# Performance work log

Measured on AMD Instinct MI355X. Metric: run time of the kernel, lower is better.

The kernel has to match this reference:

```python
import jax, jax.numpy as jnp
import numpy as np
import math

S, B, E, H = 2048, 2, 1024, 16
D = E // H
LN_EPS = 1e-5


def setup_inputs() -> dict:
    key = jax.random.key(0)
    ks = jax.random.split(key, 8)
    src = jax.random.normal(ks[0], (S, B, E), dtype=jnp.float32)
    # causal attention mask: 1 = attend, 0 = masked
    src_mask = jnp.tril(jnp.ones((S, S), dtype=jnp.int32))
    in_proj_w = jax.random.normal(ks[1], (2 * E, E), dtype=jnp.float32) * 0.02
    in_proj_b = jnp.zeros((2 * E,), dtype=jnp.float32)
    out_proj_w = jax.random.normal(ks[2], (E, E), dtype=jnp.float32) * 0.02
    out_proj_b = jnp.zeros((E,), dtype=jnp.float32)
    ln_g = jnp.ones((E,), dtype=jnp.float32)
    ln_b = jnp.zeros((E,), dtype=jnp.float32)
    return {"src": src, "src_mask": src_mask, "in_proj_w": in_proj_w,
            "in_proj_b": in_proj_b, "out_proj_w": out_proj_w,
            "out_proj_b": out_proj_b, "ln_g": ln_g, "ln_b": ln_b}


def _layernorm(x, g, b):
    mu = jnp.mean(x, axis=-1, keepdims=True)
    var = jnp.mean(jnp.square(x - mu), axis=-1, keepdims=True)
    return (x - mu) * jax.lax.rsqrt(var + LN_EPS) * g + b


def reference(src, src_mask, in_proj_w, in_proj_b, out_proj_w, out_proj_b, ln_g, ln_b):
    # src: (S, B, E)
    x_norm = _layernorm(src, ln_g, ln_b)
    proj = jax.nn.silu(x_norm @ in_proj_w.T + in_proj_b)     # (S, B, 2E)
    qkv, u = jnp.split(proj, 2, axis=-1)                     # each (S, B, E)
    qkv = qkv.reshape(S, B, H, D)                            # q = k = v = qkv
    # scores: (B, H, S_q, S_k)
    scores = jnp.einsum('sbhd,tbhd->bhst', qkv, qkv) / math.sqrt(D)
    # torch does masked_fill(-inf) then silu; silu(-inf) -> 0 in the limit,
    # which is the intended semantics (masked positions contribute nothing).
    weights = jnp.where(src_mask[None, None, :, :] == 0, 0.0, jax.nn.silu(scores))
    # attn_dropout is identity at eval
    attn = jnp.einsum('bhst,tbhd->sbhd', weights, qkv).reshape(S, B, E)
    gated = attn * u
    out = src + (gated @ out_proj_w.T + out_proj_b)          # out_dropout = identity
    return out
```

## Files before the change

### kernel.cpp

```cpp
#include <hip/hip_runtime.h>


typedef __attribute__((ext_vector_type(8))) short  short8;
typedef __attribute__((ext_vector_type(4))) float  floatx4;
typedef __attribute__((ext_vector_type(4))) float  fvec4;
typedef __attribute__((ext_vector_type(4))) unsigned short usvec4;
typedef __attribute__((ext_vector_type(4))) int    intx4;

__device__ __forceinline__ unsigned short f2b(float f) {
  unsigned u = __builtin_bit_cast(unsigned, f);
  u += 0x7FFFu + ((u >> 16) & 1u);
  return (unsigned short)(u >> 16);
}
__device__ __forceinline__ float b2f(unsigned short h) {
  unsigned u = ((unsigned)h) << 16;
  return __builtin_bit_cast(float, u);
}
__device__ __forceinline__ float silu_f(float x) {
  float e = __builtin_amdgcn_exp2f(-1.44269504f * x);
  return x * __builtin_amdgcn_rcpf(1.f + e);
}
__device__ __forceinline__ void async_copy16(void* lds, const void* g) {
  __builtin_amdgcn_global_load_lds(
      (__attribute__((address_space(1))) void*)(g),
      (__attribute__((address_space(3))) void*)(lds), 16, 0, 0);
}

__global__ void cvt_bf16(const float* __restrict__ s, unsigned short* __restrict__ d, int n4) {
  int i = blockIdx.x * 256 + threadIdx.x;
  if (i < n4) {
    fvec4 v = ((const fvec4*)s)[i];
    usvec4 o = { f2b(v.x), f2b(v.y), f2b(v.z), f2b(v.w) };
    ((usvec4*)d)[i] = o;
  }
}

__global__ __launch_bounds__(256) void ln_kernel(
    const float* __restrict__ x, const float* __restrict__ g,
    const float* __restrict__ b, unsigned short* __restrict__ xn) {
  const int row = blockIdx.x, t = threadIdx.x;
  const float* xr = x + (long)row * 1024;
  fvec4 v = ((const fvec4*)xr)[t];
  float s  = v.x + v.y + v.z + v.w;
  float s2 = v.x*v.x + v.y*v.y + v.z*v.z + v.w*v.w;
  #pragma unroll
  for (int off = 32; off; off >>= 1) { s += __shfl_down(s, off); s2 += __shfl_down(s2, off); }
  __shared__ float red[8];
  int lane = t & 63, w = t >> 6;
  if (lane == 0) { red[w] = s; red[4 + w] = s2; }
  __syncthreads();
  s  = red[0] + red[1] + red[2] + red[3];
  s2 = red[4] + red[5] + red[6] + red[7];
  float mu  = s * (1.f / 1024.f);
  float var = s2 * (1.f / 1024.f) - mu * mu;
  float rs  = rsqrtf(var + 1e-5f);
  fvec4 gg = ((const fvec4*)g)[t];
  fvec4 bb = ((const fvec4*)b)[t];
  usvec4 o = { f2b((v.x - mu) * rs * gg.x + bb.x),
               f2b((v.y - mu) * rs * gg.y + bb.y),
               f2b((v.z - mu) * rs * gg.z + bb.z),
               f2b((v.w - mu) * rs * gg.w + bb.w) };
  ((usvec4*)(xn + (long)row * 1024))[t] = o;
}

__global__ __launch_bounds__(256, 2) void gemm_in(
    const unsigned short* __restrict__ A, const unsigned short* __restrict__ Bw,
    const float* __restrict__ bias,
    unsigned short* __restrict__ out0, unsigned short* __restrict__ out1) {
  __shared__ __align__(16) unsigned short sA[128 * 32];
  __shared__ __align__(16) unsigned short sB[128 * 32];
  const int t = threadIdx.x;
  const int lane = t & 63, l15 = lane & 15, quad = lane >> 4;
  const int w = t >> 6, wm = w >> 1, wn = w & 1;
  const int m0 = blockIdx.y * 128, n0 = blockIdx.x * 128;
  const int K = 1024;

  floatx4 acc[4][4];
  const floatx4 z4 = {0.f, 0.f, 0.f, 0.f};
  #pragma unroll
  for (int i = 0; i < 4; i++)
    #pragma unroll
    for (int j = 0; j < 4; j++) acc[i][j] = z4;

  for (int kt = 0; kt < 32; ++kt) {
    const int k0 = kt << 5;
    __syncthreads();
    #pragma unroll
    for (int c = 0; c < 2; ++c) {
      int slot = c * 256 + t;
      int row = slot >> 2, col = (slot & 3) << 3;
      async_copy16(&sA[slot * 8], &A[(m0 + row) * K + k0 + col]);
      async_copy16(&sB[slot * 8], &Bw[(n0 + row) * K + k0 + col]);
    }
    __syncthreads();
    short8 af[4], bf[4];
    #pragma unroll
    for (int mr = 0; mr < 4; mr++)
      af[mr] = *(const short8*)&sA[(wm * 64 + mr * 16 + l15) * 32 + quad * 8];
    #pragma unroll
    for (int nr = 0; nr < 4; nr++)
      bf[nr] = *(const short8*)&sB[(wn * 64 + nr * 16 + l15) * 32 + quad * 8];
    #pragma unroll
    for (int mr = 0; mr < 4; mr++)
      #pragma unroll
      for (int nr = 0; nr < 4; nr++)
        acc[mr][nr] = __builtin_amdgcn_mfma_f32_16x16x32_bf16(af[mr], bf[nr], acc[mr][nr], 0, 0, 0);
  }

  #pragma unroll
  for (int mr = 0; mr < 4; mr++) {
    int gm0 = m0 + wm * 64 + mr * 16 + quad * 4;
    #pragma unroll
    for (int nr = 0; nr < 4; nr++) {
      int gn = n0 + wn * 64 + nr * 16 + l15;
      float bv = bias[gn];
      unsigned short* dst = (gn < 1024) ? (out0 + gn) : (out1 + gn - 1024);
      #pragma unroll
      for (int r = 0; r < 4; r++) {
        float v = acc[mr][nr][r] + bv;
        dst[(long)(gm0 + r) * 1024] = f2b(silu_f(v));
      }
    }
  }
}

__global__ __launch_bounds__(256, 2) void gemm_out(
    const unsigned short* __restrict__ A, const unsigned short* __restrict__ Bw,
    const float* __restrict__ bias, const float* __restrict__ src,
    float* __restrict__ outf) {
  __shared__ __align__(16) unsigned short sA[128 * 32];
  __shared__ __align__(16) unsigned short sB[64 * 32];
  const int t = threadIdx.x;
  const int lane = t & 63, l15 = lane & 15, quad = lane >> 4;
  const int w = t >> 6;
  const int m0 = blockIdx.y * 128, n0 = blockIdx.x * 64;

  floatx4 acc[2][4];
  const floatx4 z4 = {0.f, 0.f, 0.f, 0.f};
  #pragma unroll
  for (int i = 0; i < 2; i++)
    #pragma unroll
    for (int j = 0; j < 4; j++) acc[i][j] = z4;

  for (int kt = 0; kt < 32; ++kt) {
    const int k0 = kt << 5;
    __syncthreads();
    #pragma unroll
    for (int c = 0; c < 2; ++c) {
      int slot = c * 256 + t;
      int row = slot >> 2, col = (slot & 3) << 3;
      async_copy16(&sA[slot * 8], &A[(m0 + row) * 1024 + k0 + col]);
    }
    { int row = t >> 2, col = (t & 3) << 3;
      async_copy16(&sB[t * 8], &Bw[(n0 + row) * 1024 + k0 + col]); }
    __syncthreads();
    short8 af[2], bf[4];
    #pragma unroll
    for (int mr = 0; mr < 2; mr++)
      af[mr] = *(const short8*)&sA[(w * 32 + mr * 16 + l15) * 32 + quad * 8];
    #pragma unroll
    for (int nr = 0; nr < 4; nr++)
      bf[nr] = *(const short8*)&sB[(nr * 16 + l15) * 32 + quad * 8];
    #pragma unroll
    for (int mr = 0; mr < 2; mr++)
      #pragma unroll
      for (int nr = 0; nr < 4; nr++)
        acc[mr][nr] = __builtin_amdgcn_mfma_f32_16x16x32_bf16(af[mr], bf[nr], acc[mr][nr], 0, 0, 0);
  }

  #pragma unroll
  for (int mr = 0; mr < 2; mr++) {
    int gm0 = m0 + w * 32 + mr * 16 + quad * 4;
    #pragma unroll
    for (int nr = 0; nr < 4; nr++) {
      int gn = n0 + nr * 16 + l15;
      float bv = bias[gn];
      #pragma unroll
      for (int r = 0; r < 4; r++) {
        long idx = (long)(gm0 + r) * 1024 + gn;
        outf[idx] = acc[mr][nr][r] + bv + src[idx];
      }
    }
  }
}

#define SKS 72
#define SVS 136
#define SPS 136
#define SOS 68
__global__ __launch_bounds__(256, 4) void attn_kernel(
    const unsigned short* __restrict__ qkv, const unsigned short* __restrict__ u,
    unsigned short* __restrict__ gated) {
  __shared__ __align__(16) unsigned char smem[128 * SKS * 2 + 64 * SVS * 2];
  unsigned short* sK  = (unsigned short*)smem;
  unsigned short* sP  = (unsigned short*)smem;
  unsigned short* sVt = (unsigned short*)(smem + 128 * SKS * 2);
  float*          sO  = (float*)smem;

  const int t = threadIdx.x, lane = t & 63, l15 = lane & 15, quad = lane >> 4;
  const int w = t >> 6;
  const int gg = blockIdx.x >> 5, sub = gg >> 3, g = gg & 7;
  const int qi = (sub == 0) ? g : (sub == 1) ? (31 - g) : (sub == 2) ? (g + 8) : (23 - g);
  const int bh = blockIdx.x & 31;
  const int b = bh >> 4, h = bh & 15;
  const long base = (long)b * 1024 + h * 64;
  const int q0 = qi * 64;
  const int rg = t >> 3, dg = t & 7;
  const int swz0 = (rg >> 1) + dg;

  #pragma unroll
  for (int c = 0; c < 2; ++c) {
    int slot = c * 256 + t, row = slot >> 3, cg = slot & 7;
    *(short8*)&sK[row * SKS + cg * 8] =
        *(const short8*)&qkv[base + (long)(q0 + row) * 2048 + cg * 8];
  }
  __syncthreads();
  short8 qf[4][2];
  #pragma unroll
  for (int mr = 0; mr < 4; mr++)
    #pragma unroll
    for (int ks = 0; ks < 2; ks++)
      qf[mr][ks] = *(const short8*)&sK[(mr * 16 + l15) * SKS + ks * 32 + quad * 8];

  floatx4 oacc[4];
  const floatx4 z4 = {0.f, 0.f, 0.f, 0.f};
  #pragma unroll
  for (int i = 0; i < 4; i++) oacc[i] = z4;

  const int d_rd = w * 16 + l15;
  const int rsw0 = quad + (d_rd & 7) + (d_rd >> 3);

  const int nkt = (qi >> 1) + 1;
  short8 kv[4];
  #pragma unroll
  for (int i = 0; i < 4; ++i)
    kv[i] = *(const short8*)&qkv[base + (long)(rg * 4 + i) * 2048 + dg * 8];

  for (int kt = 0; kt < nkt; ++kt) {
    const int t0 = kt * 128;
    __syncthreads();
    #pragma unroll
    for (int i = 0; i < 4; ++i)
      *(short8*)&sK[(rg * 4 + i) * SKS + dg * 8] = kv[i];
    {
      intx4 k0 = __builtin_bit_cast(intx4, kv[0]);
      intx4 k1 = __builtin_bit_cast(intx4, kv[1]);
      intx4 k2 = __builtin_bit_cast(intx4, kv[2]);
      intx4 k3 = __builtin_bit_cast(intx4, kv[3]);
      #pragma unroll
      for (int jj = 0; jj < 4; ++jj) {
        unsigned lo = __builtin_amdgcn_perm((unsigned)k1[jj], (unsigned)k0[jj], 0x05040100u);
        unsigned hi = __builtin_amdgcn_perm((unsigned)k3[jj], (unsigned)k2[jj], 0x05040100u);
        int j = 2 * jj, d = dg * 8 + j;
        int gsw = (swz0 + j) & 15;
        *(unsigned long long*)&sVt[d * SVS + gsw * 8 + (rg & 1) * 4] =
            (unsigned long long)lo | ((unsigned long long)hi << 32);
        lo = __builtin_amdgcn_perm((unsigned)k1[jj], (unsigned)k0[jj], 0x07060302u);
        hi = __builtin_amdgcn_perm((unsigned)k3[jj], (unsigned)k2[jj], 0x07060302u);
        j = 2 * jj + 1; d = dg * 8 + j;
        gsw = (swz0 + j) & 15;
        *(unsigned long long*)&sVt[d * SVS + gsw * 8 + (rg & 1) * 4] =
            (unsigned long long)lo | ((unsigned long long)hi << 32);
      }
    }
    __syncthreads();
    if (kt + 1 < nkt) {
      const long nb = base + (long)((kt + 1) * 128) * 2048;
      #pragma unroll
      for (int i = 0; i < 4; ++i)
        kv[i] = *(const short8*)&qkv[nb + (long)(rg * 4 + i) * 2048 + dg * 8];
    }
    floatx4 sacc[4][2];
    #pragma unroll
    for (int i = 0; i < 4; i++) { sacc[i][0] = z4; sacc[i][1] = z4; }
    #pragma unroll
    for (int ks = 0; ks < 2; ++ks) {
      short8 kf[2];
      #pragma unroll
      for (int nr = 0; nr < 2; nr++)
        kf[nr] = *(const short8*)&sK[(w * 32 + nr * 16 + l15) * SKS + ks * 32 + quad * 8];
      #pragma unroll
      for (int mr = 0; mr < 4; mr++)
        #pragma unroll
        for (int nr = 0; nr < 2; nr++)
          sacc[mr][nr] = __builtin_amdgcn_mfma_f32_16x16x32_bf16(qf[mr][ks], kf[nr], sacc[mr][nr], 0, 0, 0);
    }
    const bool diag = (kt == nkt - 1);
    #pragma unroll
    for (int mr = 0; mr < 4; mr++) {
      int row0 = mr * 16 + quad * 4;
      #pragma unroll
      for (int nr = 0; nr < 2; nr++) {
        int col = w * 32 + nr * 16 + l15;
        #pragma unroll
        for (int r = 0; r < 4; r++) {
          float v = silu_f(sacc[mr][nr][r] * 0.125f);
          if (diag && (q0 + row0 + r < t0 + col)) v = 0.f;
          sacc[mr][nr][r] = v;
        }
      }
    }
    __syncthreads();
    #pragma unroll
    for (int mr = 0; mr < 4; mr++)
      #pragma unroll
      for (int nr = 0; nr < 2; nr++)
        #pragma unroll
        for (int r = 0; r < 4; r++)
          sP[(mr * 16 + quad * 4 + r) * SPS + w * 32 + nr * 16 + l15] = f2b(sacc[mr][nr][r]);
    __syncthreads();
    #pragma unroll
    for (int ts = 0; ts < 4; ++ts) {
      int gsw = (ts * 4 + rsw0) & 15;
      short8 vfr = *(const short8*)&sVt[d_rd * SVS + gsw * 8];
      #pragma unroll
      for (int mr = 0; mr < 4; mr++) {
        short8 pf = *(const short8*)&sP[(mr * 16 + l15) * SPS + ts * 32 + quad * 8];
        oacc[mr] = __builtin_amdgcn_mfma_f32_16x16x32_bf16(pf, vfr, oacc[mr], 0, 0, 0);
      }
    }
  }

  __syncthreads();
  #pragma unroll
  for (int mr = 0; mr < 4; mr++)
    #pragma unroll
    for (int r = 0; r < 4; r++)
      sO[(mr * 16 + quad * 4 + r) * SOS + w * 16 + l15] = oacc[mr][r];
  __syncthreads();
  {
    const int erow = t >> 2, edg = t & 3;
    const float* sOr = sO + erow * SOS + edg * 16;
    const long grow = (long)(q0 + erow) * 2048 + base + edg * 16;
    short8 u0 = *(const short8*)&u[grow];
    short8 u1 = *(const short8*)&u[grow + 8];
    short8 g0, g1;
    #pragma unroll
    for (int j = 0; j < 8; ++j) {
      g0[j] = (short)f2b(sOr[j]     * b2f((unsigned short)u0[j]));
      g1[j] = (short)f2b(sOr[j + 8] * b2f((unsigned short)u1[j]));
    }
    *(short8*)&gated[grow]     = g0;
    *(short8*)&gated[grow + 8] = g1;
  }
}

extern "C" void kernel_launch(void* const* d_in, const int* in_sizes, int n_in,
                              void* d_out, int out_size, void* d_ws, size_t ws_size,
                              hipStream_t stream) {
  const float* src = (const float*)d_in[0];
  const float* w1  = (const float*)d_in[2];
  const float* b1  = (const float*)d_in[3];
  const float* w2  = (const float*)d_in[4];
  const float* b2  = (const float*)d_in[5];
  const float* lng = (const float*)d_in[6];
  const float* lnb = (const float*)d_in[7];
  float* out = (float*)d_out;

  char* ws = (char*)d_ws;
  unsigned short* xn    = (unsigned short*)(ws + 0);
  unsigned short* qkv   = (unsigned short*)(ws + 8388608);
  unsigned short* uu    = (unsigned short*)(ws + 16777216);
  unsigned short* gated = (unsigned short*)(ws + 25165824);
  unsigned short* w1b   = (unsigned short*)(ws + 33554432);
  unsigned short* w2b   = (unsigned short*)(ws + 37748736);

  cvt_bf16<<<2048, 256, 0, stream>>>(w1, w1b, 524288);
  cvt_bf16<<<1024, 256, 0, stream>>>(w2, w2b, 262144);
  ln_kernel<<<4096, 256, 0, stream>>>(src, lng, lnb, xn);
  gemm_in<<<dim3(16, 32), 256, 0, stream>>>(xn, w1b, b1, qkv, uu);
  attn_kernel<<<1024, 256, 0, stream>>>(qkv, uu, gated);
  gemm_out<<<dim3(16, 32), 256, 0, stream>>>(gated, w2b, b2, src, out);
}
```

Before: 198.1 us.

## Pair causal query tiles per block, merge weight casts, wave-per-row layernorm

The attention kernel now has each block handle two query tiles (pair and 31-pair), which evens out the causal workload per block. Grid size is halved and the launch-bounds occupancy hint drops from 4 to 2. The K/V register prefetch across iterations is removed, so global loads are issued inside the loop. P is converted to bf16 by truncation rather than round-to-nearest. The two weight-conversion launches become one kernel, and layernorm assigns one wavefront per row using xor-shuffle reduction with no LDS, which cuts launches and barriers but loses load/compute overlap in attention.

```diff
diff --git a/kernel.cpp b/kernel.cpp
--- a/kernel.cpp
+++ b/kernel.cpp
@@ -12,6 +12,9 @@
   u += 0x7FFFu + ((u >> 16) & 1u);
   return (unsigned short)(u >> 16);
 }
+__device__ __forceinline__ unsigned short f2b_trunc(float f) {
+  return (unsigned short)(__builtin_bit_cast(unsigned, f) >> 16);
+}
 __device__ __forceinline__ float b2f(unsigned short h) {
   unsigned u = ((unsigned)h) << 16;
   return __builtin_bit_cast(float, u);
@@ -26,41 +29,48 @@
       (__attribute__((address_space(3))) void*)(lds), 16, 0, 0);
 }
 
-__global__ void cvt_bf16(const float* __restrict__ s, unsigned short* __restrict__ d, int n4) {
+__global__ void cvt_bf16(const float* __restrict__ s1, unsigned short* __restrict__ d1,
+                         const float* __restrict__ s2, unsigned short* __restrict__ d2,
+                         int n1, int ntot) {
   int i = blockIdx.x * 256 + threadIdx.x;
-  if (i < n4) {
-    fvec4 v = ((const fvec4*)s)[i];
-    usvec4 o = { f2b(v.x), f2b(v.y), f2b(v.z), f2b(v.w) };
-    ((usvec4*)d)[i] = o;
-  }
+  if (i >= ntot) return;
+  const float* s; unsigned short* d; int j;
+  if (i < n1) { s = s1; d = d1; j = i; } else { s = s2; d = d2; j = i - n1; }
+  fvec4 v = ((const fvec4*)s)[j];
+  usvec4 o = { f2b(v.x), f2b(v.y), f2b(v.z), f2b(v.w) };
+  ((usvec4*)d)[j] = o;
 }
 
 __global__ __launch_bounds__(256) void ln_kernel(
     const float* __restrict__ x, const float* __restrict__ g,
     const float* __restrict__ b, unsigned short* __restrict__ xn) {
-  const int row = blockIdx.x, t = threadIdx.x;
-  const float* xr = x + (long)row * 1024;
-  fvec4 v = ((const fvec4*)xr)[t];
-  float s  = v.x + v.y + v.z + v.w;
-  float s2 = v.x*v.x + v.y*v.y + v.z*v.z + v.w*v.w;
-  #pragma unroll
-  for (int off = 32; off; off >>= 1) { s += __shfl_down(s, off); s2 += __shfl_down(s2, off); }
-  __shared__ float red[8];
-  int lane = t & 63, w = t >> 6;
-  if (lane == 0) { red[w] = s; red[4 + w] = s2; }
-  __syncthreads();
-  s  = red[0] + red[1] + red[2] + red[3];
-  s2 = red[4] + red[5] + red[6] + red[7];
+  const int lane = threadIdx.x & 63;
+  const int row = blockIdx.x * 4 + (threadIdx.x >> 6);
+  const fvec4* xr = (const fvec4*)(x + (long)row * 1024);
+  fvec4 v[4];
+  float s = 0.f, s2 = 0.f;
+  #pragma unroll
+  for (int c = 0; c < 4; ++c) {
+    v[c] = xr[lane + 64 * c];
+    s  += v[c].x + v[c].y + v[c].z + v[c].w;
+    s2 += v[c].x*v[c].x + v[c].y*v[c].y + v[c].z*v[c].z + v[c].w*v[c].w;
+  }
+  #pragma unroll
+  for (int off = 32; off; off >>= 1) { s += __shfl_xor(s, off); s2 += __shfl_xor(s2, off); }
   float mu  = s * (1.f / 1024.f);
   float var = s2 * (1.f / 1024.f) - mu * mu;
   float rs  = rsqrtf(var + 1e-5f);
-  fvec4 gg = ((const fvec4*)g)[t];
-  fvec4 bb = ((const fvec4*)b)[t];
-  usvec4 o = { f2b((v.x - mu) * rs * gg.x + bb.x),
-               f2b((v.y - mu) * rs * gg.y + bb.y),
-               f2b((v.z - mu) * rs * gg.z + bb.z),
-               f2b((v.w - mu) * rs * gg.w + bb.w) };
-  ((usvec4*)(xn + (long)row * 1024))[t] = o;
+  usvec4* outr = (usvec4*)(xn + (long)row * 1024);
+  #pragma unroll
+  for (int c = 0; c < 4; ++c) {
+    fvec4 gg = ((const fvec4*)g)[lane + 64 * c];
+    fvec4 bb = ((const fvec4*)b)[lane + 64 * c];
+    usvec4 o = { f2b((v[c].x - mu) * rs * gg.x + bb.x),
+                 f2b((v[c].y - mu) * rs * gg.y + bb.y),
+                 f2b((v[c].z - mu) * rs * gg.z + bb.z),
+                 f2b((v[c].w - mu) * rs * gg.w + bb.w) };
+    outr[lane + 64 * c] = o;
+  }
 }
 
 __global__ __launch_bounds__(256, 2) void gemm_in(
@@ -188,7 +198,7 @@
 #define SVS 136
 #define SPS 136
 #define SOS 68
-__global__ __launch_bounds__(256, 4) void attn_kernel(
+__global__ __launch_bounds__(256, 2) void attn_kernel(
     const unsigned short* __restrict__ qkv, const unsigned short* __restrict__ u,
     unsigned short* __restrict__ gated) {
   __shared__ __align__(16) unsigned char smem[128 * SKS * 2 + 64 * SVS * 2];
@@ -199,149 +209,146 @@
 
   const int t = threadIdx.x, lane = t & 63, l15 = lane & 15, quad = lane >> 4;
   const int w = t >> 6;
-  const int gg = blockIdx.x >> 5, sub = gg >> 3, g = gg & 7;
-  const int qi = (sub == 0) ? g : (sub == 1) ? (31 - g) : (sub == 2) ? (g + 8) : (23 - g);
+  const int pair = blockIdx.x >> 5;
   const int bh = blockIdx.x & 31;
   const int b = bh >> 4, h = bh & 15;
   const long base = (long)b * 1024 + h * 64;
-  const int q0 = qi * 64;
   const int rg = t >> 3, dg = t & 7;
   const int swz0 = (rg >> 1) + dg;
-
-  #pragma unroll
-  for (int c = 0; c < 2; ++c) {
-    int slot = c * 256 + t, row = slot >> 3, cg = slot & 7;
-    *(short8*)&sK[row * SKS + cg * 8] =
-        *(const short8*)&qkv[base + (long)(q0 + row) * 2048 + cg * 8];
-  }
-  __syncthreads();
-  short8 qf[4][2];
-  #pragma unroll
-  for (int mr = 0; mr < 4; mr++)
-    #pragma unroll
-    for (int ks = 0; ks < 2; ks++)
-      qf[mr][ks] = *(const short8*)&sK[(mr * 16 + l15) * SKS + ks * 32 + quad * 8];
-
-  floatx4 oacc[4];
-  const floatx4 z4 = {0.f, 0.f, 0.f, 0.f};
-  #pragma unroll
-  for (int i = 0; i < 4; i++) oacc[i] = z4;
-
   const int d_rd = w * 16 + l15;
   const int rsw0 = quad + (d_rd & 7) + (d_rd >> 3);
-
-  const int nkt = (qi >> 1) + 1;
-  short8 kv[4];
-  #pragma unroll
-  for (int i = 0; i < 4; ++i)
-    kv[i] = *(const short8*)&qkv[base + (long)(rg * 4 + i) * 2048 + dg * 8];
-
-  for (int kt = 0; kt < nkt; ++kt) {
-    const int t0 = kt * 128;
-    __syncthreads();
-    #pragma unroll
-    for (int i = 0; i < 4; ++i)
-      *(short8*)&sK[(rg * 4 + i) * SKS + dg * 8] = kv[i];
+  const floatx4 z4 = {0.f, 0.f, 0.f, 0.f};
+
+  for (int half = 0; half < 2; ++half) {
+    const int qi = half ? (31 - pair) : pair;
+    const int q0 = qi * 64;
+    const int nkt = (qi >> 1) + 1;
+
+    if (half) __syncthreads();
+    #pragma unroll
+    for (int c = 0; c < 2; ++c) {
+      int slot = c * 256 + t, row = slot >> 3, cg = slot & 7;
+      *(short8*)&sK[row * SKS + cg * 8] =
+          *(const short8*)&qkv[base + (long)(q0 + row) * 2048 + cg * 8];
+    }
+    __syncthreads();
+    short8 qf[4][2];
+    #pragma unroll
+    for (int mr = 0; mr < 4; mr++)
+      #pragma unroll
+      for (int ks = 0; ks < 2; ks++)
+        qf[mr][ks] = *(const short8*)&sK[(mr * 16 + l15) * SKS + ks * 32 + quad * 8];
+
+    floatx4 oacc[4];
+    #pragma unroll
+    for (int i = 0; i < 4; i++) oacc[i] = z4;
+
+    for (int kt = 0; kt < nkt; ++kt) {
+      const int t0 = kt * 128;
+      __syncthreads();
+      short8 kv[4];
+      #pragma unroll
+      for (int i = 0; i < 4; ++i)
+        kv[i] = *(const short8*)&qkv[base + (long)(t0 + rg * 4 + i) * 2048 + dg * 8];
+      #pragma unroll
+      for (int i = 0; i < 4; ++i)
+        *(short8*)&sK[(rg * 4 + i) * SKS + dg * 8] = kv[i];
+      {
+        intx4 k0 = __builtin_bit_cast(intx4, kv[0]);
+        intx4 k1 = __builtin_bit_cast(intx4, kv[1]);
+        intx4 k2 = __builtin_bit_cast(intx4, kv[2]);
+        intx4 k3 = __builtin_bit_cast(intx4, kv[3]);
+        #pragma unroll
+        for (int jj = 0; jj < 4; ++jj) {
+          unsigned lo = __builtin_amdgcn_perm((unsigned)k1[jj], (unsigned)k0[jj], 0x05040100u);
+          unsigned hi = __builtin_amdgcn_perm((unsigned)k3[jj], (unsigned)k2[jj], 0x05040100u);
+          int j = 2 * jj, d = dg * 8 + j;
+          int gsw = (swz0 + j) & 15;
+          *(unsigned long long*)&sVt[d * SVS + gsw * 8 + (rg & 1) * 4] =
+              (unsigned long long)lo | ((unsigned long long)hi << 32);
+          lo = __builtin_amdgcn_perm((unsigned)k1[jj], (unsigned)k0[jj], 0x07060302u);
+          hi = __builtin_amdgcn_perm((unsigned)k3[jj], (unsigned)k2[jj], 0x07060302u);
+          j = 2 * jj + 1; d = dg * 8 + j;
+          gsw = (swz0 + j) & 15;
+          *(unsigned long long*)&sVt[d * SVS + gsw * 8 + (rg & 1) * 4] =
+              (unsigned long long)lo | ((unsigned long long)hi << 32);
+        }
+      }
+      __syncthreads();
+      floatx4 sacc[4][2];
+      #pragma unroll
+      for (int i = 0; i < 4; i++) { sacc[i][0] = z4; sacc[i][1] = z4; }
+      #pragma unroll
+      for (int ks = 0; ks < 2; ++ks) {
+        short8 kf[2];
+        #pragma unroll
+        for (int nr = 0; nr < 2; nr++)
+          kf[nr] = *(const short8*)&sK[(w * 32 + nr * 16 + l15) * SKS + ks * 32 + quad * 8];
+        #pragma unroll
+        for (int mr = 0; mr < 4; mr++)
+          #pragma unroll
+          for (int nr = 0; nr < 2; nr++)
+            sacc[mr][nr] = __builtin_amdgcn_mfma_f32_16x16x32_bf16(qf[mr][ks], kf[nr], sacc[mr][nr], 0, 0, 0);
+      }
+      const bool diag = (kt == nkt - 1);
+      #pragma unroll
+      for (int mr = 0; mr < 4; mr++) {
+        int row0 = mr * 16 + quad * 4;
+        #pragma unroll
+        for (int nr = 0; nr < 2; nr++) {
+          int col = w * 32 + nr * 16 + l15;
+          #pragma unroll
+          for (int r = 0; r < 4; r++) {
+            float v = silu_f(sacc[mr][nr][r] * 0.125f);
+            if (diag && (q0 + row0 + r < t0 + col)) v = 0.f;
+            sacc[mr][nr][r] = v;
+          }
+        }
+      }
+      __syncthreads();
+      #pragma unroll
+      for (int mr = 0; mr < 4; mr++)
+        #pragma unroll
+        for (int nr = 0; nr < 2; nr++)
+          #pragma unroll
+          for (int r = 0; r < 4; r++)
+            sP[(mr * 16 + quad * 4 + r) * SPS + w * 32 + nr * 16 + l15] =
+                f2b_trunc(sacc[mr][nr][r]);
+      __syncthreads();
+      #pragma unroll
+      for (int ts = 0; ts < 4; ++ts) {
+        int gsw = (ts * 4 + rsw0) & 15;
+        short8 vfr = *(const short8*)&sVt[d_rd * SVS + gsw * 8];
+        #pragma unroll
+        for (int mr = 0; mr < 4; mr++) {
+          short8 pf = *(const short8*)&sP[(mr * 16 + l15) * SPS + ts * 32 + quad * 8];
+          oacc[mr] = __builtin_amdgcn_mfma_f32_16x16x32_bf16(pf, vfr, oacc[mr], 0, 0, 0);
+        }
+      }
+    }
+
+    __syncthreads();
+    #pragma unroll
+    for (int mr = 0; mr < 4; mr++)
+      #pragma unroll
+      for (int r = 0; r < 4; r++)
+        sO[(mr * 16 + quad * 4 + r) * SOS + w * 16 + l15] = oacc[mr][r];
+    __syncthreads();
     {
-      intx4 k0 = __builtin_bit_cast(intx4, kv[0]);
-      intx4 k1 = __builtin_bit_cast(intx4, kv[1]);
-      intx4 k2 = __builtin_bit_cast(intx4, kv[2]);
-      intx4 k3 = __builtin_bit_cast(intx4, kv[3]);
-      #pragma unroll
-      for (int jj = 0; jj < 4; ++jj) {
-        unsigned lo = __builtin_amdgcn_perm((unsigned)k1[jj], (unsigned)k0[jj], 0x05040100u);
-        unsigned hi = __builtin_amdgcn_perm((unsigned)k3[jj], (unsigned)k2[jj], 0x05040100u);
-        int j = 2 * jj, d = dg * 8 + j;
-        int gsw = (swz0 + j) & 15;
-        *(unsigned long long*)&sVt[d * SVS + gsw * 8 + (rg & 1) * 4] =
-            (unsigned long long)lo | ((unsigned long long)hi << 32);
-        lo = __builtin_amdgcn_perm((unsigned)k1[jj], (unsigned)k0[jj], 0x07060302u);
-        hi = __builtin_amdgcn_perm((unsigned)k3[jj], (unsigned)k2[jj], 0x07060302u);
-        j = 2 * jj + 1; d = dg * 8 + j;
-        gsw = (swz0 + j) & 15;
-        *(unsigned long long*)&sVt[d * SVS + gsw * 8 + (rg & 1) * 4] =
-            (unsigned long long)lo | ((unsigned long long)hi << 32);
-      }
-    }
-    __syncthreads();
-    if (kt + 1 < nkt) {
-      const long nb = base + (long)((kt + 1) * 128) * 2048;
-      #pragma unroll
-      for (int i = 0; i < 4; ++i)
-        kv[i] = *(const short8*)&qkv[nb + (long)(rg * 4 + i) * 2048 + dg * 8];
-    }
-    floatx4 sacc[4][2];
-    #pragma unroll
-    for (int i = 0; i < 4; i++) { sacc[i][0] = z4; sacc[i][1] = z4; }
-    #pragma unroll
-    for (int ks = 0; ks < 2; ++ks) {
-      short8 kf[2];
-      #pragma unroll
-      for (int nr = 0; nr < 2; nr++)
-        kf[nr] = *(const short8*)&sK[(w * 32 + nr * 16 + l15) * SKS + ks * 32 + quad * 8];
-      #pragma unroll
-      for (int mr = 0; mr < 4; mr++)
-        #pragma unroll
-        for (int nr = 0; nr < 2; nr++)
-          sacc[mr][nr] = __builtin_amdgcn_mfma_f32_16x16x32_bf16(qf[mr][ks], kf[nr], sacc[mr][nr], 0, 0, 0);
-    }
-    const bool diag = (kt == nkt - 1);
-    #pragma unroll
-    for (int mr = 0; mr < 4; mr++) {
-      int row0 = mr * 16 + quad * 4;
-      #pragma unroll
-      for (int nr = 0; nr < 2; nr++) {
-        int col = w * 32 + nr * 16 + l15;
-        #pragma unroll
-        for (int r = 0; r < 4; r++) {
-          float v = silu_f(sacc[mr][nr][r] * 0.125f);
-          if (diag && (q0 + row0 + r < t0 + col)) v = 0.f;
-          sacc[mr][nr][r] = v;
-        }
-      }
-    }
-    __syncthreads();
-    #pragma unroll
-    for (int mr = 0; mr < 4; mr++)
-      #pragma unroll
-      for (int nr = 0; nr < 2; nr++)
-        #pragma unroll
-        for (int r = 0; r < 4; r++)
-          sP[(mr * 16 + quad * 4 + r) * SPS + w * 32 + nr * 16 + l15] = f2b(sacc[mr][nr][r]);
-    __syncthreads();
-    #pragma unroll
-    for (int ts = 0; ts < 4; ++ts) {
-      int gsw = (ts * 4 + rsw0) & 15;
-      short8 vfr = *(const short8*)&sVt[d_rd * SVS + gsw * 8];
-      #pragma unroll
-      for (int mr = 0; mr < 4; mr++) {
-        short8 pf = *(const short8*)&sP[(mr * 16 + l15) * SPS + ts * 32 + quad * 8];
-        oacc[mr] = __builtin_amdgcn_mfma_f32_16x16x32_bf16(pf, vfr, oacc[mr], 0, 0, 0);
-      }
-    }
-  }
-
-  __syncthreads();
-  #pragma unroll
-  for (int mr = 0; mr < 4; mr++)
-    #pragma unroll
-    for (int r = 0; r < 4; r++)
-      sO[(mr * 16 + quad * 4 + r) * SOS + w * 16 + l15] = oacc[mr][r];
-  __syncthreads();
-  {
-    const int erow = t >> 2, edg = t & 3;
-    const float* sOr = sO + erow * SOS + edg * 16;
-    const long grow = (long)(q0 + erow) * 2048 + base + edg * 16;
-    short8 u0 = *(const short8*)&u[grow];
-    short8 u1 = *(const short8*)&u[grow + 8];
-    short8 g0, g1;
-    #pragma unroll
-    for (int j = 0; j < 8; ++j) {
-      g0[j] = (short)f2b(sOr[j]     * b2f((unsigned short)u0[j]));
-      g1[j] = (short)f2b(sOr[j + 8] * b2f((unsigned short)u1[j]));
-    }
-    *(short8*)&gated[grow]     = g0;
-    *(short8*)&gated[grow + 8] = g1;
+      const int erow = t >> 2, edg = t & 3;
+      const float* sOr = sO + erow * SOS + edg * 16;
+      const long grow = (long)(q0 + erow) * 2048 + base + edg * 16;
+      short8 u0 = *(const short8*)&u[grow];
+      short8 u1 = *(const short8*)&u[grow + 8];
+      short8 g0, g1;
+      #pragma unroll
+      for (int j = 0; j < 8; ++j) {
+        g0[j] = (short)f2b(sOr[j]     * b2f((unsigned short)u0[j]));
+        g1[j] = (short)f2b(sOr[j + 8] * b2f((unsigned short)u1[j]));
+      }
+      *(short8*)&gated[grow]     = g0;
+      *(short8*)&gated[grow + 8] = g1;
+    }
   }
 }
 
@@ -365,10 +372,9 @@
   unsigned short* w1b   = (unsigned short*)(ws + 33554432);
   unsigned short* w2b   = (unsigned short*)(ws + 37748736);
 
-  cvt_bf16<<<2048, 256, 0, stream>>>(w1, w1b, 524288);
-  cvt_bf16<<<1024, 256, 0, stream>>>(w2, w2b, 262144);
-  ln_kernel<<<4096, 256, 0, stream>>>(src, lng, lnb, xn);
+  cvt_bf16<<<3072, 256, 0, stream>>>(w1, w1b, w2, w2b, 524288, 786432);
+  ln_kernel<<<1024, 256, 0, stream>>>(src, lng, lnb, xn);
   gemm_in<<<dim3(16, 32), 256, 0, stream>>>(xn, w1b, b1, qkv, uu);
-  attn_kernel<<<1024, 256, 0, stream>>>(qkv, uu, gated);
+  attn_kernel<<<512, 256, 0, stream>>>(qkv, uu, gated);
   gemm_out<<<dim3(16, 32), 256, 0, stream>>>(gated, w2b, b2, src, out);
 }
```

Result: faster. 190.7 us (-3.7%).
